# Kernel tuning notes

Hardware: AMD Instinct MI355X
Metric: run time of the kernel (lower is better)

The kernel has to match this reference:

```python
import jax, jax.numpy as jnp
import numpy as np

HEADS = 20  # head_dim = 1280 / 20 = 64, SD convention


def setup_inputs() -> dict:
    key = jax.random.key(0)
    ks = jax.random.split(key, 6)
    B, S, D = 2, 2048, 1280
    scale = 1.0 / np.sqrt(D)
    return {
        "hidden_states": jax.random.normal(ks[0], (B, S, D), dtype=jnp.float32),
        "Wq": jax.random.normal(ks[1], (D, D), dtype=jnp.float32) * scale,
        "Wk": jax.random.normal(ks[2], (D, D), dtype=jnp.float32) * scale,
        "Wv": jax.random.normal(ks[3], (D, D), dtype=jnp.float32) * scale,
        "Wo": jax.random.normal(ks[4], (D, D), dtype=jnp.float32) * scale,
        "bo": jnp.zeros((D,), dtype=jnp.float32),
    }


def reference(hidden_states, Wq, Wk, Wv, Wo, bo):
    B, S, D = hidden_states.shape
    H = HEADS
    hd = D // H
    sm_scale = 1.0 / jnp.sqrt(jnp.asarray(hd, dtype=hidden_states.dtype))

    # unfused QKV projections (to_q / to_k / to_v, no bias in diffusers default)
    q = hidden_states @ Wq  # [B, S, D]
    k = hidden_states @ Wk
    v = hidden_states @ Wv

    # head_to_batch_dim: [B, S, D] -> [B, H, S, hd]
    def split_heads(x):
        return x.reshape(B, S, H, hd).transpose(0, 2, 1, 3)

    q, k, v = split_heads(q), split_heads(k), split_heads(v)

    # get_attention_scores: scaled QK^T then softmax (full matrix materialized)
    scores = jnp.einsum("bhqd,bhkd->bhqk", q, k) * sm_scale  # [B, H, S, S]
    probs = jax.nn.softmax(scores, axis=-1)

    # probs @ V, then batch_to_head_dim: [B, H, S, hd] -> [B, S, D]
    out = jnp.einsum("bhqk,bhkd->bhqd", probs, v)
    out = out.transpose(0, 2, 1, 3).reshape(B, S, D)

    # to_out[0] linear (with bias) + to_out[1] dropout (identity at inference)
    out = out @ Wo + bo
    return out
```

## Files before the change

kernel.cpp:

```cpp
#include <hip/hip_runtime.h>
#include <hip/hip_bf16.h>

typedef __bf16 bf16x8 __attribute__((ext_vector_type(8)));
typedef float  f32x4  __attribute__((ext_vector_type(4)));
typedef float  f32x16 __attribute__((ext_vector_type(16)));

#define H_  20
#define S_  2048
#define D_  1280
#define HD_ 64
#define M_  4096

__device__ __forceinline__ unsigned short f2bf(float f) {
    union { float f; unsigned int u; } v; v.f = f;
    return (unsigned short)((v.u + 0x7FFFu + ((v.u >> 16) & 1u)) >> 16);
}

__device__ __forceinline__ unsigned short b2u(float f) {
    union { __bf16 b; unsigned short u; } v; v.b = (__bf16)f; return v.u;
}

__device__ __forceinline__ float fexp2(float x) {
    return __builtin_amdgcn_exp2f(x);
}

__device__ __forceinline__ unsigned cvtpk(float lo, float hi) {
    unsigned r;
    asm("v_cvt_pk_bf16_f32 %0, %1, %2" : "=v"(r) : "v"(lo), "v"(hi));
    return r;
}

__device__ __forceinline__ void gll16(const void* g, void* l) {
    __builtin_amdgcn_global_load_lds(
        (const __attribute__((address_space(1))) unsigned int*)g,
        (__attribute__((address_space(3))) unsigned int*)l, 16, 0, 0);
}

#define WAIT_BAR(N) asm volatile("s_waitcnt vmcnt(" #N ")\n\ts_barrier" ::: "memory")

#define SWZ(base, row, g) \
    (*(const bf16x8*)((base) + (row) * 64 + (((g) ^ ((row) & 7)) * 8)))

#define SWZG(base, row, g) \
    (*(const bf16x8*)((base) + (row) * 32 + ((((g) ^ (((row) >> 1) & 3)) * 8))))

__global__ __launch_bounds__(256) void cast_bf16_kernel(
    const float* __restrict__ in, unsigned short* __restrict__ out, int n)
{
    int i = (blockIdx.x * 256 + threadIdx.x) * 4;
    if (i + 3 < n) {
        const float4 v = *(const float4*)(in + i);
        ushort4 o;
        o.x = f2bf(v.x); o.y = f2bf(v.y); o.z = f2bf(v.z); o.w = f2bf(v.w);
        *(ushort4*)(out + i) = o;
    }
}

__global__ __launch_bounds__(256) void transpose_cast_kernel(
    const float* __restrict__ W0, const float* __restrict__ W1,
    const float* __restrict__ W2, const float* __restrict__ W3,
    unsigned short* __restrict__ outbase)
{
    __shared__ unsigned short tile[64][65];
    const float* src = (blockIdx.z == 0) ? W0 : (blockIdx.z == 1) ? W1 :
                       (blockIdx.z == 2) ? W2 : W3;
    unsigned short* dst = outbase + (size_t)blockIdx.z * D_ * D_;
    int n0 = blockIdx.x * 64, k0 = blockIdx.y * 64;
    int tx = threadIdx.x & 63, ty = threadIdx.x >> 6;
#pragma unroll
    for (int i = 0; i < 16; ++i) {
        int row = ty * 16 + i;
        tile[row][tx] = f2bf(src[(size_t)(k0 + row) * D_ + n0 + tx]);
    }
    __syncthreads();
#pragma unroll
    for (int i = 0; i < 16; ++i) {
        int row = ty * 16 + i;
        dst[(size_t)(n0 + row) * D_ + k0 + tx] = tile[tx][row];
    }
}

__global__ __launch_bounds__(256) void gemm_bf16(
    const unsigned short* __restrict__ A, const unsigned short* __restrict__ Bt,
    void* __restrict__ C0, void* __restrict__ C1, void* __restrict__ C2,
    const float* __restrict__ bias,
    int Kdim, int Ndim, int mode, float oscale)
{
    __shared__ unsigned short sh[24576];
    const int t = threadIdx.x;
    const int wid = t >> 6, lane = t & 63;

    const int lin = blockIdx.x + blockIdx.y * gridDim.x;
    const int xcd = lin & 7, q = lin >> 3;
    const int bx = q >> 2, by = xcd * 4 + (q & 3);

    const int m0 = by * 128, n0 = bx * 128;
    const int wm = (wid >> 1) * 64, wn = (wid & 1) * 64;
    const int ln15 = lane & 15, ln4 = lane >> 4;

    f32x4 acc[4][4];
#pragma unroll
    for (int i = 0; i < 4; ++i)
#pragma unroll
        for (int j = 0; j < 4; ++j) acc[i][j] = (f32x4){0.f, 0.f, 0.f, 0.f};

    const int r0 = t >> 2;
    const int c0s = (((t & 3) ^ ((r0 >> 1) & 3)) * 8);
    const unsigned short* Ab = A + (size_t)m0 * Kdim;
    const unsigned short* Bb = Bt + (size_t)n0 * Kdim;
    const int nk = Kdim >> 5;

#define STAGE_G(k0, Abuf, Bbuf)                                           \
    do {                                                                  \
        gll16(Ab + (size_t)(r0) * Kdim + (k0) + c0s,      (Abuf) + wid * 512);        \
        gll16(Ab + (size_t)(64 + r0) * Kdim + (k0) + c0s, (Abuf) + 2048 + wid * 512); \
        gll16(Bb + (size_t)(r0) * Kdim + (k0) + c0s,      (Bbuf) + wid * 512);        \
        gll16(Bb + (size_t)(64 + r0) * Kdim + (k0) + c0s, (Bbuf) + 2048 + wid * 512); \
    } while (0)

    unsigned short *A0 = sh, *A1 = sh + 4096, *A2 = sh + 8192;
    unsigned short *B0 = sh + 12288, *B1 = sh + 16384, *B2 = sh + 20480;

    STAGE_G(0, A0, B0);
    STAGE_G(32, A1, B1);
    WAIT_BAR(4);

    for (int kk = 0; kk < nk; ++kk) {
        if (kk + 2 < nk) STAGE_G((kk + 2) << 5, A2, B2);

        bf16x8 af[4], bfr[4];
#pragma unroll
        for (int i = 0; i < 4; ++i) af[i]  = SWZG(A0, wm + i * 16 + ln15, ln4);
#pragma unroll
        for (int i = 0; i < 4; ++i) bfr[i] = SWZG(B0, wn + i * 16 + ln15, ln4);
#pragma unroll
        for (int i = 0; i < 4; ++i)
#pragma unroll
            for (int j = 0; j < 4; ++j)
                acc[i][j] = __builtin_amdgcn_mfma_f32_16x16x32_bf16(af[i], bfr[j], acc[i][j], 0, 0, 0);

        if (kk + 1 < nk) {
            if (kk + 2 < nk) WAIT_BAR(4);
            else             WAIT_BAR(0);
        }
        unsigned short* tA = A0; A0 = A1; A1 = A2; A2 = tA;
        unsigned short* tB = B0; B0 = B1; B1 = B2; B2 = tB;
    }
#undef STAGE_G

#pragma unroll
    for (int i = 0; i < 4; ++i) {
#pragma unroll
        for (int j = 0; j < 4; ++j) {
            const int gmb = m0 + wm + i * 16 + ln4 * 4;
            const int gn  = n0 + wn + j * 16 + ln15;
#pragma unroll
            for (int r = 0; r < 4; ++r) {
                float val = acc[i][j][r];
                const int m = gmb + r;
                const int b = m >> 11, s = m & 2047;
                if (mode == 3) {
                    ((float*)C0)[(size_t)m * Ndim + gn] = val + bias[gn];
                } else {
                    const int which = gn / 1280;
                    const int nn = gn - which * 1280;
                    const int h = nn >> 6, d = nn & 63;
                    if (which == 0) val *= oscale;
                    size_t idx;
                    void* dst;
                    if (which == 2) { idx = ((size_t)(b * H_ + h) * HD_ + d) * S_ + s; dst = C2; }
                    else            { idx = ((size_t)(b * H_ + h) * S_ + s) * HD_ + d; dst = (which == 0) ? C0 : C1; }
                    ((unsigned short*)dst)[idx] = f2bf(val);
                }
            }
        }
    }
}

template<int NSPLIT>
__global__ __launch_bounds__(256) void attn_kernel(
    const unsigned short* __restrict__ Q, const unsigned short* __restrict__ K,
    const unsigned short* __restrict__ V, unsigned short* __restrict__ O,
    float* __restrict__ Op, float* __restrict__ Ml)
{
    __shared__ unsigned short lds[16384];

    const int t = threadIdx.x, wid = t >> 6, lane = t & 63;
    const int ln31 = lane & 31, lhi = lane >> 5;

    int qtile, bh, split;
    if constexpr (NSPLIT == 2) {
        const int lin = blockIdx.x + blockIdx.y * 32;
        const int nl  = (lin & 7) * 160 + (lin >> 3);
        split = nl & 1; qtile = (nl >> 1) & 15; bh = nl >> 5;
    } else {
        const int lin = blockIdx.x + blockIdx.y * 16;
        const int nl  = (lin & 7) * 80 + (lin >> 3);
        split = 0; qtile = nl & 15; bh = nl >> 4;
    }

    const int q0 = qtile * 128;
    const int t00 = split * 1024;
    const int NT  = (NSPLIT == 2) ? 16 : 32;
    const unsigned short* Qh = Q + (size_t)bh * S_ * HD_;
    const unsigned short* Kh = K + (size_t)bh * S_ * HD_;
    const unsigned short* Vh = V + (size_t)bh * HD_ * S_;

    const int srow = t >> 3;
    const int scol = (((t & 7) ^ (srow & 7)) * 8);

#pragma unroll
    for (int j = 0; j < 4; ++j)
        gll16(Qh + (size_t)(q0 + j * 32 + srow) * HD_ + scol,
              lds + 8192 + j * 2048 + wid * 512);
    __syncthreads();

    bf16x8 qf[4];
    {
        const int row = wid * 32 + ln31;
#pragma unroll
        for (int j = 0; j < 4; ++j)
            qf[j] = SWZ(lds + 8192, row, j * 2 + lhi);
    }

    gll16(Kh + (size_t)(t00 + srow) * HD_ + scol,      lds + wid * 512);
    gll16(Kh + (size_t)(t00 + 32 + srow) * HD_ + scol, lds + 2048 + wid * 512);
    gll16(Vh + (size_t)srow * S_ + t00 + scol,         lds + 4096 + wid * 512);
    gll16(Vh + (size_t)(32 + srow) * S_ + t00 + scol,  lds + 4096 + 2048 + wid * 512);
    __syncthreads();

    const unsigned short* Kp = Kh + (size_t)(t00 + 64 + srow) * HD_ + scol;
    const unsigned short* Vp = Vh + (size_t)srow * S_ + t00 + 64 + scol;

    f32x16 ot[2];
#pragma unroll
    for (int r = 0; r < 16; ++r) { ot[0][r] = 0.f; ot[1][r] = 0.f; }
    float m_ = -3.0e38f, l_ = 0.f;

    for (int it = 0; it < NT; ++it) {
        const unsigned short* cb = lds + (it & 1) * 8192;
        if (it + 1 < NT) {
            unsigned short* nb = lds + ((it + 1) & 1) * 8192;
            gll16(Kp,            nb + wid * 512);
            gll16(Kp + 32 * HD_, nb + 2048 + wid * 512);
            gll16(Vp,            nb + 4096 + wid * 512);
            gll16(Vp + 32 * S_,  nb + 4096 + 2048 + wid * 512);
            Kp += 64 * HD_;
            Vp += 64;
        }

        f32x16 st[2];
#pragma unroll
        for (int r = 0; r < 16; ++r) { st[0][r] = 0.f; st[1][r] = 0.f; }
        __builtin_amdgcn_s_setprio(1);
#pragma unroll
        for (int h = 0; h < 2; ++h) {
            const int row = h * 32 + ln31;
#pragma unroll
            for (int j = 0; j < 4; ++j) {
                const bf16x8 kf = SWZ(cb, row, j * 2 + lhi);
                st[h] = __builtin_amdgcn_mfma_f32_32x32x16_bf16(kf, qf[j], st[h], 0, 0, 0);
            }
        }
        __builtin_amdgcn_s_setprio(0);

        float t8[8];
#pragma unroll
        for (int i = 0; i < 8; ++i)
            t8[i] = fmaxf(fmaxf(st[0][i], st[0][i + 8]), fmaxf(st[1][i], st[1][i + 8]));
        const float ta = fmaxf(fmaxf(t8[0], t8[4]), fmaxf(t8[1], t8[5]));
        const float tb = fmaxf(fmaxf(t8[2], t8[6]), fmaxf(t8[3], t8[7]));
        float rm = fmaxf(ta, tb);
        rm = fmaxf(rm, __shfl_xor(rm, 32));

        if (__any(rm - m_ > 8.0f)) {
            const float mn = fmaxf(m_, rm);
            const float sf = fexp2(m_ - mn);
            l_ *= sf;
#pragma unroll
            for (int r = 0; r < 16; ++r) { ot[0][r] *= sf; ot[1][r] *= sf; }
            m_ = mn;
        }

#pragma unroll
        for (int r = 0; r < 16; ++r) {
            st[0][r] = fexp2(st[0][r] - m_);
            st[1][r] = fexp2(st[1][r] - m_);
        }

        {
            float s8[8];
#pragma unroll
            for (int i = 0; i < 8; ++i)
                s8[i] = (st[0][i] + st[0][i + 8]) + (st[1][i] + st[1][i + 8]);
#pragma unroll
            for (int i = 0; i < 4; ++i) s8[i] += s8[i + 4];
            float rs = (s8[0] + s8[1]) + (s8[2] + s8[3]);
            rs += __shfl_xor(rs, 32);
            l_ += rs;
        }

        bf16x8 pa[4];
#pragma unroll
        for (int c = 0; c < 4; ++c) {
            const int hh = c >> 1, rb = (c & 1) * 8;
            const unsigned wA = cvtpk(st[hh][rb + 0], st[hh][rb + 1]);
            const unsigned wB = cvtpk(st[hh][rb + 2], st[hh][rb + 3]);
            const unsigned wC = cvtpk(st[hh][rb + 4], st[hh][rb + 5]);
            const unsigned wD = cvtpk(st[hh][rb + 6], st[hh][rb + 7]);
            auto s0 = __builtin_amdgcn_permlane32_swap(wA, wC, false, false);
            auto s1 = __builtin_amdgcn_permlane32_swap(wB, wD, false, false);
            union { unsigned i[4]; bf16x8 v; } u;
            u.i[0] = s0[0]; u.i[1] = s1[0]; u.i[2] = s0[1]; u.i[3] = s1[1];
            pa[c] = u.v;
        }

        __builtin_amdgcn_s_setprio(1);
#pragma unroll
        for (int h = 0; h < 2; ++h) {
            const int row = h * 32 + ln31;
#pragma unroll
            for (int c = 0; c < 4; ++c) {
                const bf16x8 vf = SWZ(cb + 4096, row, c * 2 + lhi);
                ot[h] = __builtin_amdgcn_mfma_f32_32x32x16_bf16(vf, pa[c], ot[h], 0, 0, 0);
            }
        }
        __builtin_amdgcn_s_setprio(0);

        __syncthreads();
    }

    const int qloc = wid * 32 + ln31;
    const int qg = q0 + qloc;

    if constexpr (NSPLIT == 2) {
        const size_t rowi = (size_t)(split * 40 + bh) * 2048 + qg;
        if (lhi == 0) {
            float2 s; s.x = m_; s.y = l_;
            ((float2*)Ml)[rowi] = s;
        }
        float* Orow = Op + rowi * 64;
#pragma unroll
        for (int h = 0; h < 2; ++h)
#pragma unroll
            for (int g = 0; g < 4; ++g) {
                f32x4 w = {ot[h][g * 4 + 0], ot[h][g * 4 + 1],
                           ot[h][g * 4 + 2], ot[h][g * 4 + 3]};
                *(f32x4*)(Orow + h * 32 + lhi * 4 + g * 8) = w;
            }
    } else {
        const int b = bh / H_, hh = bh % H_;
        const float inv = 1.0f / l_;
        unsigned short* Orow = O + (size_t)(b * S_ + qg) * D_ + hh * HD_;
#pragma unroll
        for (int h = 0; h < 2; ++h)
#pragma unroll
            for (int g = 0; g < 4; ++g) {
                ushort4 w;
                w.x = b2u(ot[h][g * 4 + 0] * inv);
                w.y = b2u(ot[h][g * 4 + 1] * inv);
                w.z = b2u(ot[h][g * 4 + 2] * inv);
                w.w = b2u(ot[h][g * 4 + 3] * inv);
                *(ushort4*)(Orow + h * 32 + lhi * 4 + g * 8) = w;
            }
    }
}

__global__ __launch_bounds__(256) void attn_combine(
    const float* __restrict__ Op, const float* __restrict__ Ml,
    unsigned short* __restrict__ O)
{
    const int gid = blockIdx.x * 256 + threadIdx.x;
    const int row = gid >> 4;
    const int c   = (gid & 15) * 4;
    const int bh = row >> 11, qg = row & 2047;

    const float2 s0 = ((const float2*)Ml)[row];
    const float2 s1 = ((const float2*)Ml)[81920 + row];
    const float mm = fmaxf(s0.x, s1.x);
    const float a0 = fexp2(s0.x - mm), a1 = fexp2(s1.x - mm);
    const float inv = 1.0f / (a0 * s0.y + a1 * s1.y);

    const f32x4 o0 = *(const f32x4*)(Op + (size_t)row * 64 + c);
    const f32x4 o1 = *(const f32x4*)(Op + (size_t)(81920 + row) * 64 + c);

    const int b = bh / H_, hh = bh % H_;
    ushort4 w;
    w.x = b2u((a0 * o0[0] + a1 * o1[0]) * inv);
    w.y = b2u((a0 * o0[1] + a1 * o1[1]) * inv);
    w.z = b2u((a0 * o0[2] + a1 * o1[2]) * inv);
    w.w = b2u((a0 * o0[3] + a1 * o1[3]) * inv);
    *(ushort4*)(O + (size_t)(b * S_ + qg) * D_ + hh * HD_ + c) = w;
}

extern "C" void kernel_launch(void* const* d_in, const int* in_sizes, int n_in,
                              void* d_out, int out_size, void* d_ws, size_t ws_size,
                              hipStream_t stream)
{
    const float* hid = (const float*)d_in[0];
    const float* Wq  = (const float*)d_in[1];
    const float* Wk  = (const float*)d_in[2];
    const float* Wv  = (const float*)d_in[3];
    const float* Wo  = (const float*)d_in[4];
    const float* bo  = (const float*)d_in[5];
    float* out = (float*)d_out;

    char* ws = (char*)d_ws;
    unsigned short* Xb  = (unsigned short*)(ws);
    unsigned short* Wt  = (unsigned short*)(ws + 10485760);
    unsigned short* Qb  = (unsigned short*)(ws + 23592960);
    unsigned short* Kb  = (unsigned short*)(ws + 34078720);
    unsigned short* Vb  = (unsigned short*)(ws + 44564480);
    unsigned short* Ob  = (unsigned short*)(ws + 55050240);
    float*          Opart = (float*)(ws + 65536000);
    float*          Mpart = (float*)(ws + 107479040);
    const size_t ws_need = 108789760ull;

    cast_bf16_kernel<<<5120, 256, 0, stream>>>(hid, Xb, M_ * D_);
    transpose_cast_kernel<<<dim3(20, 20, 4), 256, 0, stream>>>(Wq, Wk, Wv, Wo, Wt);

    const float SCALE_Q = 0.125f * 1.44269504088896340736f;

    gemm_bf16<<<dim3(30, 32), 256, 0, stream>>>(Xb, Wt, Qb, Kb, Vb, nullptr,
                                                D_, 3840, 4, SCALE_Q);

    if (ws_size >= ws_need) {
        attn_kernel<2><<<dim3(32, 40), 256, 0, stream>>>(Qb, Kb, Vb, Ob, Opart, Mpart);
        attn_combine<<<5120, 256, 0, stream>>>(Opart, Mpart, Ob);
    } else {
        attn_kernel<1><<<dim3(16, 40), 256, 0, stream>>>(Qb, Kb, Vb, Ob, nullptr, nullptr);
    }

    gemm_bf16<<<dim3(10, 32), 256, 0, stream>>>(Ob, Wt + 3 * 1638400, out, nullptr, nullptr, bo,
                                                D_, D_, 3, 1.0f);
}
```

Measured before the change: 187.9 us.

## Triple-buffer K/V tiles and software-pipeline QK^T ahead of softmax-PV

Replaces the double-buffered attention loop with a three-stage LDS ring buffer, prefetching K/V two tiles ahead and using partial vmcnt waits. The QK^T MFMAs for the next tile are issued before the softmax and PV of the current tile, so matrix work can overlap the exponentials and reductions. The cost is 48KB of LDS instead of 32KB and a second set of score registers, both of which can lower occupancy.

```diff
diff --git a/kernel.cpp b/kernel.cpp
--- a/kernel.cpp
+++ b/kernel.cpp
@@ -37,6 +37,7 @@
 }
 
 #define WAIT_BAR(N) asm volatile("s_waitcnt vmcnt(" #N ")\n\ts_barrier" ::: "memory")
+#define BAR_FENCE() asm volatile("s_barrier" ::: "memory")
 
 #define SWZ(base, row, g) \
     (*(const bf16x8*)((base) + (row) * 64 + (((g) ^ ((row) & 7)) * 8)))
@@ -183,7 +184,7 @@
     const unsigned short* __restrict__ V, unsigned short* __restrict__ O,
     float* __restrict__ Op, float* __restrict__ Ml)
 {
-    __shared__ unsigned short lds[16384];
+    __shared__ unsigned short lds[24576];
 
     const int t = threadIdx.x, wid = t >> 6, lane = t & 63;
     const int ln31 = lane & 31, lhi = lane >> 5;
@@ -212,7 +213,7 @@
 #pragma unroll
     for (int j = 0; j < 4; ++j)
         gll16(Qh + (size_t)(q0 + j * 32 + srow) * HD_ + scol,
-              lds + 8192 + j * 2048 + wid * 512);
+              lds + 16384 + j * 2048 + wid * 512);
     __syncthreads();
 
     bf16x8 qf[4];
@@ -220,118 +221,131 @@
         const int row = wid * 32 + ln31;
 #pragma unroll
         for (int j = 0; j < 4; ++j)
-            qf[j] = SWZ(lds + 8192, row, j * 2 + lhi);
+            qf[j] = SWZ(lds + 16384, row, j * 2 + lhi);
     }
 
     gll16(Kh + (size_t)(t00 + srow) * HD_ + scol,      lds + wid * 512);
     gll16(Kh + (size_t)(t00 + 32 + srow) * HD_ + scol, lds + 2048 + wid * 512);
     gll16(Vh + (size_t)srow * S_ + t00 + scol,         lds + 4096 + wid * 512);
     gll16(Vh + (size_t)(32 + srow) * S_ + t00 + scol,  lds + 4096 + 2048 + wid * 512);
+    gll16(Kh + (size_t)(t00 + 64 + srow) * HD_ + scol,      lds + 8192 + wid * 512);
+    gll16(Kh + (size_t)(t00 + 96 + srow) * HD_ + scol,      lds + 8192 + 2048 + wid * 512);
+    gll16(Vh + (size_t)srow * S_ + t00 + 64 + scol,         lds + 8192 + 4096 + wid * 512);
+    gll16(Vh + (size_t)(32 + srow) * S_ + t00 + 64 + scol,  lds + 8192 + 4096 + 2048 + wid * 512);
     __syncthreads();
 
-    const unsigned short* Kp = Kh + (size_t)(t00 + 64 + srow) * HD_ + scol;
-    const unsigned short* Vp = Vh + (size_t)srow * S_ + t00 + 64 + scol;
+    const unsigned short* Kp = Kh + (size_t)(t00 + 128 + srow) * HD_ + scol;
+    const unsigned short* Vp = Vh + (size_t)srow * S_ + t00 + 128 + scol;
 
     f32x16 ot[2];
 #pragma unroll
     for (int r = 0; r < 16; ++r) { ot[0][r] = 0.f; ot[1][r] = 0.f; }
     float m_ = -3.0e38f, l_ = 0.f;
 
-    for (int it = 0; it < NT; ++it) {
-        const unsigned short* cb = lds + (it & 1) * 8192;
-        if (it + 1 < NT) {
-            unsigned short* nb = lds + ((it + 1) & 1) * 8192;
-            gll16(Kp,            nb + wid * 512);
-            gll16(Kp + 32 * HD_, nb + 2048 + wid * 512);
-            gll16(Vp,            nb + 4096 + wid * 512);
-            gll16(Vp + 32 * S_,  nb + 4096 + 2048 + wid * 512);
-            Kp += 64 * HD_;
-            Vp += 64;
-        }
-
-        f32x16 st[2];
-#pragma unroll
-        for (int r = 0; r < 16; ++r) { st[0][r] = 0.f; st[1][r] = 0.f; }
-        __builtin_amdgcn_s_setprio(1);
-#pragma unroll
-        for (int h = 0; h < 2; ++h) {
-            const int row = h * 32 + ln31;
-#pragma unroll
-            for (int j = 0; j < 4; ++j) {
-                const bf16x8 kf = SWZ(cb, row, j * 2 + lhi);
-                st[h] = __builtin_amdgcn_mfma_f32_32x32x16_bf16(kf, qf[j], st[h], 0, 0, 0);
-            }
-        }
-        __builtin_amdgcn_s_setprio(0);
-
-        float t8[8];
-#pragma unroll
-        for (int i = 0; i < 8; ++i)
-            t8[i] = fmaxf(fmaxf(st[0][i], st[0][i + 8]), fmaxf(st[1][i], st[1][i + 8]));
-        const float ta = fmaxf(fmaxf(t8[0], t8[4]), fmaxf(t8[1], t8[5]));
-        const float tb = fmaxf(fmaxf(t8[2], t8[6]), fmaxf(t8[3], t8[7]));
-        float rm = fmaxf(ta, tb);
-        rm = fmaxf(rm, __shfl_xor(rm, 32));
-
-        if (__any(rm - m_ > 8.0f)) {
-            const float mn = fmaxf(m_, rm);
-            const float sf = fexp2(m_ - mn);
-            l_ *= sf;
-#pragma unroll
-            for (int r = 0; r < 16; ++r) { ot[0][r] *= sf; ot[1][r] *= sf; }
-            m_ = mn;
-        }
-
-#pragma unroll
-        for (int r = 0; r < 16; ++r) {
-            st[0][r] = fexp2(st[0][r] - m_);
-            st[1][r] = fexp2(st[1][r] - m_);
-        }
-
-        {
-            float s8[8];
-#pragma unroll
-            for (int i = 0; i < 8; ++i)
-                s8[i] = (st[0][i] + st[0][i + 8]) + (st[1][i] + st[1][i + 8]);
-#pragma unroll
-            for (int i = 0; i < 4; ++i) s8[i] += s8[i + 4];
-            float rs = (s8[0] + s8[1]) + (s8[2] + s8[3]);
-            rs += __shfl_xor(rs, 32);
-            l_ += rs;
-        }
-
-        bf16x8 pa[4];
-#pragma unroll
-        for (int c = 0; c < 4; ++c) {
-            const int hh = c >> 1, rb = (c & 1) * 8;
-            const unsigned wA = cvtpk(st[hh][rb + 0], st[hh][rb + 1]);
-            const unsigned wB = cvtpk(st[hh][rb + 2], st[hh][rb + 3]);
-            const unsigned wC = cvtpk(st[hh][rb + 4], st[hh][rb + 5]);
-            const unsigned wD = cvtpk(st[hh][rb + 6], st[hh][rb + 7]);
-            auto s0 = __builtin_amdgcn_permlane32_swap(wA, wC, false, false);
-            auto s1 = __builtin_amdgcn_permlane32_swap(wB, wD, false, false);
-            union { unsigned i[4]; bf16x8 v; } u;
-            u.i[0] = s0[0]; u.i[1] = s1[0]; u.i[2] = s0[1]; u.i[3] = s1[1];
-            pa[c] = u.v;
-        }
-
-        __builtin_amdgcn_s_setprio(1);
-#pragma unroll
-        for (int h = 0; h < 2; ++h) {
-            const int row = h * 32 + ln31;
-#pragma unroll
-            for (int c = 0; c < 4; ++c) {
-                const bf16x8 vf = SWZ(cb + 4096, row, c * 2 + lhi);
-                ot[h] = __builtin_amdgcn_mfma_f32_32x32x16_bf16(vf, pa[c], ot[h], 0, 0, 0);
-            }
-        }
-        __builtin_amdgcn_s_setprio(0);
-
-        __syncthreads();
-    }
-
-    const int qloc = wid * 32 + ln31;
-    const int qg = q0 + qloc;
+    f32x16 Sa[2], Sb[2];
+
+#define QKT(SS, kbase) do {                                                      \
+    _Pragma("unroll")                                                            \
+    for (int r_ = 0; r_ < 16; ++r_) { SS[0][r_] = 0.f; SS[1][r_] = 0.f; }        \
+    _Pragma("unroll")                                                            \
+    for (int h_ = 0; h_ < 2; ++h_) {                                             \
+        const int row_ = h_ * 32 + ln31;                                         \
+        _Pragma("unroll")                                                        \
+        for (int j_ = 0; j_ < 4; ++j_) {                                         \
+            const bf16x8 kf_ = SWZ((kbase), row_, j_ * 2 + lhi);                 \
+            SS[h_] = __builtin_amdgcn_mfma_f32_32x32x16_bf16(kf_, qf[j_], SS[h_], 0, 0, 0); \
+        }                                                                        \
+    }                                                                            \
+} while (0)
+
+#define SMPV(SS, tt_) do {                                                       \
+    float t8_[8];                                                                \
+    _Pragma("unroll")                                                            \
+    for (int i_ = 0; i_ < 8; ++i_)                                               \
+        t8_[i_] = fmaxf(fmaxf(SS[0][i_], SS[0][i_ + 8]), fmaxf(SS[1][i_], SS[1][i_ + 8])); \
+    const float ta_ = fmaxf(fmaxf(t8_[0], t8_[4]), fmaxf(t8_[1], t8_[5]));       \
+    const float tb_ = fmaxf(fmaxf(t8_[2], t8_[6]), fmaxf(t8_[3], t8_[7]));       \
+    float rm_ = fmaxf(ta_, tb_);                                                 \
+    rm_ = fmaxf(rm_, __shfl_xor(rm_, 32));                                       \
+    if (__any(rm_ - m_ > 8.0f)) {                                                \
+        const float mn_ = fmaxf(m_, rm_);                                        \
+        const float sf_ = fexp2(m_ - mn_);                                       \
+        l_ *= sf_;                                                               \
+        _Pragma("unroll")                                                        \
+        for (int r_ = 0; r_ < 16; ++r_) { ot[0][r_] *= sf_; ot[1][r_] *= sf_; }  \
+        m_ = mn_;                                                                \
+    }                                                                            \
+    _Pragma("unroll")                                                            \
+    for (int r_ = 0; r_ < 16; ++r_) {                                            \
+        SS[0][r_] = fexp2(SS[0][r_] - m_);                                       \
+        SS[1][r_] = fexp2(SS[1][r_] - m_);                                       \
+    }                                                                            \
+    bf16x8 pa_[4];                                                               \
+    _Pragma("unroll")                                                            \
+    for (int c_ = 0; c_ < 4; ++c_) {                                             \
+        const int hh_ = c_ >> 1, rb_ = (c_ & 1) * 8;                             \
+        const unsigned wA_ = cvtpk(SS[hh_][rb_ + 0], SS[hh_][rb_ + 1]);          \
+        const unsigned wB_ = cvtpk(SS[hh_][rb_ + 2], SS[hh_][rb_ + 3]);          \
+        const unsigned wC_ = cvtpk(SS[hh_][rb_ + 4], SS[hh_][rb_ + 5]);          \
+        const unsigned wD_ = cvtpk(SS[hh_][rb_ + 6], SS[hh_][rb_ + 7]);          \
+        auto s0_ = __builtin_amdgcn_permlane32_swap(wA_, wC_, false, false);     \
+        auto s1_ = __builtin_amdgcn_permlane32_swap(wB_, wD_, false, false);     \
+        union { unsigned i[4]; bf16x8 v; } u_;                                   \
+        u_.i[0] = s0_[0]; u_.i[1] = s1_[0]; u_.i[2] = s0_[1]; u_.i[3] = s1_[1];  \
+        pa_[c_] = u_.v;                                                          \
+    }                                                                            \
+    const unsigned short* Vb_ = lds + ((tt_) % 3) * 8192 + 4096;                 \
+    __builtin_amdgcn_s_setprio(1);                                               \
+    _Pragma("unroll")                                                            \
+    for (int h_ = 0; h_ < 2; ++h_) {                                             \
+        const int row_ = h_ * 32 + ln31;                                         \
+        _Pragma("unroll")                                                        \
+        for (int c_ = 0; c_ < 4; ++c_) {                                         \
+            const bf16x8 vf_ = SWZ(Vb_, row_, c_ * 2 + lhi);                     \
+            ot[h_] = __builtin_amdgcn_mfma_f32_32x32x16_bf16(vf_, pa_[c_], ot[h_], 0, 0, 0); \
+        }                                                                        \
+    }                                                                            \
+    __builtin_amdgcn_s_setprio(0);                                               \
+    float s8_[8];                                                                \
+    _Pragma("unroll")                                                            \
+    for (int i_ = 0; i_ < 8; ++i_)                                               \
+        s8_[i_] = (SS[0][i_] + SS[0][i_ + 8]) + (SS[1][i_] + SS[1][i_ + 8]);     \
+    _Pragma("unroll")                                                            \
+    for (int i_ = 0; i_ < 4; ++i_) s8_[i_] += s8_[i_ + 4];                       \
+    float rs_ = (s8_[0] + s8_[1]) + (s8_[2] + s8_[3]);                           \
+    rs_ += __shfl_xor(rs_, 32);                                                  \
+    l_ += rs_;                                                                   \
+} while (0)
+
+#define STEP(SP, SN, tt_) do {                                                   \
+    if ((tt_) + 2 < NT) {                                                        \
+        unsigned short* nb_ = lds + (((tt_) + 2) % 3) * 8192;                    \
+        gll16(Kp,            nb_ + wid * 512);                                   \
+        gll16(Kp + 32 * HD_, nb_ + 2048 + wid * 512);                            \
+        gll16(Vp,            nb_ + 4096 + wid * 512);                            \
+        gll16(Vp + 32 * S_,  nb_ + 4096 + 2048 + wid * 512);                     \
+        Kp += 64 * HD_; Vp += 64;                                                \
+        WAIT_BAR(4);                                                             \
+    } else {                                                                     \
+        WAIT_BAR(0);                                                             \
+    }                                                                            \
+    if ((tt_) + 1 < NT) QKT(SN, lds + (((tt_) + 1) % 3) * 8192);                 \
+    SMPV(SP, tt_);                                                               \
+    BAR_FENCE();                                                                 \
+} while (0)
+
+    QKT(Sa, lds);
+
+    for (int tt = 0; tt < NT; tt += 2) {
+        STEP(Sa, Sb, tt);
+        STEP(Sb, Sa, tt + 1);
+    }
+
+#undef STEP
+#undef SMPV
+#undef QKT
+
+    const int qg = q0 + wid * 32 + ln31;
 
     if constexpr (NSPLIT == 2) {
         const size_t rowi = (size_t)(split * 40 + bh) * 2048 + qg;
```

After: 190.6 us. Within noise of the previous version (+1.5%).
